# Performance work log

Hardware: AMD Instinct MI355X
Metric: run time of the kernel (lower is better)

The kernel has to match this reference:

```python
import math
import jax, jax.numpy as jnp
import numpy as np

NUM_HEADS = 8
FACTOR = 5


def setup_inputs() -> dict:
    key = jax.random.key(0)
    ks = jax.random.split(key, 5)
    B, S, D = 8, 2048, 512
    s = 1.0 / math.sqrt(D)
    return {
        "x": jax.random.normal(ks[0], (B, S, D), dtype=jnp.float32),
        "wq": jax.random.normal(ks[1], (D, D), dtype=jnp.float32) * s,
        "bq": jnp.zeros((D,), jnp.float32),
        "wk": jax.random.normal(ks[2], (D, D), dtype=jnp.float32) * s,
        "bk": jnp.zeros((D,), jnp.float32),
        "wv": jax.random.normal(ks[3], (D, D), dtype=jnp.float32) * s,
        "bv": jnp.zeros((D,), jnp.float32),
        "wo": jax.random.normal(ks[4], (D, D), dtype=jnp.float32) * s,
        "bo": jnp.zeros((D,), jnp.float32),
    }


def reference(x, wq, bq, wk, bk, wv, bv, wo, bo):
    B, S, Dm = x.shape
    H = NUM_HEADS
    Dh = Dm // H
    scale = jnp.sqrt(jnp.float32(Dh))
    # u = min(factor * ceil(ln(S)), S); S is static so compute in Python
    u = min(FACTOR * int(math.ceil(math.log(S))), S)

    def split_heads(t):  # [B,S,Dm] -> [B,H,S,Dh]
        return t.reshape(B, S, H, Dh).transpose(0, 2, 1, 3)

    q = split_heads(x @ wq + bq)
    k = split_heads(x @ wk + bk)
    v = split_heads(x @ wv + bv)

    # S >= 64 -> sparse branch (static decision).
    # Full logits only to compute sparsity measure M (max - mean over keys).
    logits = jnp.einsum("bhqd,bhkd->bhqk", q, k) / scale  # [B,H,S,S]
    M = jnp.max(logits, axis=-1) - jnp.mean(logits, axis=-1)  # [B,H,S]
    _, top_idx = jax.lax.top_k(M, u)  # [B,H,u]

    # Gather top-u queries and run dense attention only for them.
    q_top = jnp.take_along_axis(q, top_idx[..., None], axis=2)  # [B,H,u,Dh]
    top_logits = jnp.einsum("bhqd,bhkd->bhqk", q_top, k) / scale  # [B,H,u,S]
    top_w = jax.nn.softmax(top_logits, axis=-1)
    top_out = jnp.einsum("bhqk,bhkd->bhqd", top_w, v)  # [B,H,u,Dh]

    # Non-selected queries get the mean of V; scatter top outputs in.
    out = jnp.broadcast_to(jnp.mean(v, axis=2, keepdims=True), v.shape)
    b_idx = jnp.arange(B)[:, None, None]
    h_idx = jnp.arange(H)[None, :, None]
    out = out.at[b_idx, h_idx, top_idx].set(top_out)  # [B,H,S,Dh]

    out = out.transpose(0, 2, 1, 3).reshape(B, S, Dm)
    return out @ wo + bo
```

## Files before the change

### kernel.cpp

```cpp
#include <hip/hip_runtime.h>
#include <hip/hip_bf16.h>
#include <math.h>

#define NB 8
#define NS 2048
#define ND 512
#define NH 8
#define DHD 64
#define NU 40
#define NBH 64
#define NM 16384

typedef __attribute__((ext_vector_type(8))) short short8;
typedef __attribute__((ext_vector_type(4))) short short4v;
typedef __attribute__((ext_vector_type(4))) float f32x4;

__device__ __forceinline__ short f2bf(float f) {
  __hip_bfloat16 h = __float2bfloat16(f);
  return *reinterpret_cast<short*>(&h);
}
__device__ __forceinline__ float bf2f(short s) {
  __hip_bfloat16 h;
  *reinterpret_cast<short*>(&h) = s;
  return __bfloat162float(h);
}

__device__ __forceinline__ void gload_lds16(const short* g, short* l) {
  __builtin_amdgcn_global_load_lds(
      (const __attribute__((address_space(1))) unsigned int*)g,
      (__attribute__((address_space(3))) unsigned int*)l, 16, 0, 0);
}

__global__ void prep(const float* __restrict__ x, const float* __restrict__ w0,
                     const float* __restrict__ w1, const float* __restrict__ w2,
                     short* __restrict__ Xs, short* __restrict__ Wts) {
  if (blockIdx.x < 8192) {
    int i = blockIdx.x * 256 + threadIdx.x;
    const float4 v = *(const float4*)(x + (size_t)i * 4);
    int row = i >> 7;
    int col = (i & 127) << 2;
    float vv[4] = {v.x, v.y, v.z, v.w};
    short4v hi, lo;
#pragma unroll
    for (int j = 0; j < 4; ++j) {
      short h = f2bf(vv[j]);
      hi[j] = h;
      lo[j] = f2bf(vv[j] - bf2f(h));
    }
    *(short4v*)(Xs + (size_t)row * 1024 + col) = hi;
    *(short4v*)(Xs + (size_t)row * 1024 + 512 + col) = lo;
  } else {
    int bw = blockIdx.x - 8192;
    int y = bw >> 8;
    int bxy = bw & 255;
    const float* W = y == 0 ? w0 : y == 1 ? w1 : w2;
    short* dst = Wts + (size_t)y * 512 * 1024;
    __shared__ float tile[32][33];
    int bx = bxy & 15, by = bxy >> 4;
    int k0 = bx * 32, n0 = by * 32;
    int r = threadIdx.x >> 3, cg = (threadIdx.x & 7) * 4;
    const float4 v = *(const float4*)(W + (size_t)(k0 + r) * 512 + n0 + cg);
    tile[r][cg] = v.x; tile[r][cg + 1] = v.y; tile[r][cg + 2] = v.z; tile[r][cg + 3] = v.w;
    __syncthreads();
#pragma unroll
    for (int j = 0; j < 4; ++j) {
      int kk = cg + j;
      float f = tile[kk][r];
      short h = f2bf(f);
      dst[(size_t)(n0 + r) * 1024 + k0 + kk] = h;
      dst[(size_t)(n0 + r) * 1024 + 512 + k0 + kk] = f2bf(f - bf2f(h));
    }
  }
}

__global__ __launch_bounds__(256, 2) void qkvgemm(
    const short* __restrict__ A, const short* __restrict__ Wts,
    const float* __restrict__ bq, const float* __restrict__ bk,
    const float* __restrict__ bv, short* __restrict__ Qs,
    short* __restrict__ Ks, short* __restrict__ Vs) {
  __shared__ short As[2][128][64];
  __shared__ short Bs[2][128][64];
  const int bid = blockIdx.x;
  const int wgid = (bid & 7) * 192 + (bid >> 3);
  const int mb = wgid / 12, y = wgid % 12;
  const int m0 = mb * 128;
  const int wsel = y >> 2;
  const int n0 = (y & 3) * 128;
  const short* Wb = Wts + (size_t)wsel * 512 * 1024;
  const float* bias = wsel == 0 ? bq : wsel == 1 ? bk : bv;
  short* dstbase = wsel == 0 ? Qs : wsel == 1 ? Ks : Vs;

  const int tid = threadIdx.x;
  const int w = tid >> 6, lane = tid & 63;
  const int wm = (w >> 1) * 64, wn = (w & 1) * 64;
  const int fr = lane & 15, fk = lane >> 4;

  f32x4 acc[4][4];
  const f32x4 zz = {0.f, 0.f, 0.f, 0.f};
#pragma unroll
  for (int i = 0; i < 4; ++i)
#pragma unroll
    for (int j = 0; j < 4; ++j) acc[i][j] = zz;

  auto stage = [&](int buf, int kt) {
#pragma unroll
    for (int p = 0; p < 4; ++p) {
      int idx = (p * 4 + w) * 64 + lane;
      int r = idx >> 3, c = idx & 7;
      int cs = c ^ (r & 7);
      int sc = (cs < 4) ? (kt + cs * 8) : (512 + kt + (cs - 4) * 8);
      short* lA = &As[buf][0][0] + (p * 4 + w) * 512;
      short* lB = &Bs[buf][0][0] + (p * 4 + w) * 512;
      gload_lds16(A + (size_t)(m0 + r) * 1024 + sc, lA);
      gload_lds16(Wb + (size_t)(n0 + r) * 1024 + sc, lB);
    }
  };

  stage(0, 0);
  __syncthreads();
  for (int kt = 0; kt < 512; kt += 32) {
    int cur = (kt >> 5) & 1;
    if (kt + 32 < 512) stage(cur ^ 1, kt + 32);
    short8 ah[4], al[4], bh[4], bl[4];
#pragma unroll
    for (int mf = 0; mf < 4; ++mf) {
      int r = wm + mf * 16 + fr;
      ah[mf] = *(const short8*)&As[cur][r][(fk ^ (r & 7)) << 3];
      al[mf] = *(const short8*)&As[cur][r][((4 + fk) ^ (r & 7)) << 3];
    }
#pragma unroll
    for (int nf = 0; nf < 4; ++nf) {
      int r = wn + nf * 16 + fr;
      bh[nf] = *(const short8*)&Bs[cur][r][(fk ^ (r & 7)) << 3];
      bl[nf] = *(const short8*)&Bs[cur][r][((4 + fk) ^ (r & 7)) << 3];
    }
#pragma unroll
    for (int mf = 0; mf < 4; ++mf)
#pragma unroll
      for (int nf = 0; nf < 4; ++nf) {
        acc[mf][nf] = __builtin_amdgcn_mfma_f32_16x16x32_bf16(bh[nf], ah[mf], acc[mf][nf], 0, 0, 0);
        acc[mf][nf] = __builtin_amdgcn_mfma_f32_16x16x32_bf16(bh[nf], al[mf], acc[mf][nf], 0, 0, 0);
        acc[mf][nf] = __builtin_amdgcn_mfma_f32_16x16x32_bf16(bl[nf], ah[mf], acc[mf][nf], 0, 0, 0);
      }
    __syncthreads();
  }

#pragma unroll
  for (int mf = 0; mf < 4; ++mf) {
    int m = m0 + wm + mf * 16 + fr;
    int b = m >> 11, s = m & 2047;
#pragma unroll
    for (int nf = 0; nf < 4; ++nf) {
      int nb = n0 + wn + nf * 16 + fk * 4;
      float4 bi4 = *(const float4*)(bias + nb);
      int h = nb >> 6, dh = nb & 63;
      short* dst = dstbase + ((size_t)((b << 3) + h) * 2048 + s) * 128;
      short4v hi, lo;
      float bb[4] = {bi4.x, bi4.y, bi4.z, bi4.w};
#pragma unroll
      for (int j = 0; j < 4; ++j) {
        float v = acc[mf][nf][j] + bb[j];
        short hs = f2bf(v);
        hi[j] = hs;
        lo[j] = f2bf(v - bf2f(hs));
      }
      *(short4v*)(dst + dh) = hi;
      *(short4v*)(dst + 64 + dh) = lo;
    }
  }
}

__global__ __launch_bounds__(256) void colmeans(const short* __restrict__ K,
                                                const short* __restrict__ V,
                                                float* __restrict__ kbarf,
                                                float* __restrict__ vbarf) {
  const int bh = blockIdx.x >> 2, part = blockIdx.x & 3;
  const int c = threadIdx.x & 15;
  const int g = threadIdx.x >> 4;
  const int s0 = part * 512 + g * 32;
  const short* Kb = K + (size_t)bh * 2048 * 128;
  const short* Vb = V + (size_t)bh * 2048 * 128;
  float sk[8], sv[8];
#pragma unroll
  for (int e = 0; e < 8; ++e) { sk[e] = 0.f; sv[e] = 0.f; }
  for (int s = s0; s < s0 + 32; ++s) {
    short8 k8 = *(const short8*)(Kb + (size_t)s * 128 + c * 8);
    short8 v8 = *(const short8*)(Vb + (size_t)s * 128 + c * 8);
#pragma unroll
    for (int e = 0; e < 8; ++e) { sk[e] += bf2f(k8[e]); sv[e] += bf2f(v8[e]); }
  }
  __shared__ float rk[16][128], rv[16][128];
#pragma unroll
  for (int e = 0; e < 8; ++e) { rk[g][c * 8 + e] = sk[e]; rv[g][c * 8 + e] = sv[e]; }
  __syncthreads();
  if (threadIdx.x < 64) {
    int d = threadIdx.x;
    float a = 0.f, b2 = 0.f;
    for (int g2 = 0; g2 < 16; ++g2) {
      a += rk[g2][d] + rk[g2][64 + d];
      b2 += rv[g2][d] + rv[g2][64 + d];
    }
    atomicAdd(kbarf + bh * 64 + d, a * (1.f / 2048.f));
    atomicAdd(vbarf + bh * 64 + d, b2 * (1.f / 2048.f));
  }
}

__global__ __launch_bounds__(256, 2) void qkmax(const short* __restrict__ Qs,
                                                const short* __restrict__ Ks,
                                                const float* __restrict__ kbarf,
                                                float* __restrict__ Mval) {
  __shared__ short Kt[2][128][128];
  __shared__ float red[256];
  const int bid = blockIdx.x;
  const int wgid = (bid & 7) * 64 + (bid >> 3);
  const int bh = wgid >> 3, q0 = (wgid & 7) * 256;
  const short* Qb = Qs + ((size_t)bh * 2048 + q0) * 128;
  const short* Kb = Ks + (size_t)bh * 2048 * 128;
  const int tid = threadIdx.x, w = tid >> 6, lane = tid & 63;
  const int fr = lane & 15, fk = lane >> 4;

  short8 qf[4][2][2];
#pragma unroll
  for (int mf = 0; mf < 4; ++mf) {
    int row = w * 64 + mf * 16 + fr;
#pragma unroll
    for (int h = 0; h < 2; ++h)
#pragma unroll
      for (int k0 = 0; k0 < 2; ++k0) {
        int ch = h * 8 + k0 * 4 + fk;
        qf[mf][h][k0] = *(const short8*)(Qb + (size_t)row * 128 + ch * 8);
      }
  }

  f32x4 rmax[4];
  const f32x4 neg = {-1e30f, -1e30f, -1e30f, -1e30f};
#pragma unroll
  for (int mf = 0; mf < 4; ++mf) rmax[mf] = neg;
  const f32x4 zz = {0.f, 0.f, 0.f, 0.f};

  auto stageK = [&](int buf, int t) {
#pragma unroll
    for (int p = 0; p < 8; ++p) {
      int idx = (p * 4 + w) * 64 + lane;
      int r = idx >> 4, c = idx & 15;
      int cs = c ^ (r & 15);
      short* lb = &Kt[buf][0][0] + (p * 4 + w) * 512;
      gload_lds16(Kb + (size_t)(t * 128 + r) * 128 + cs * 8, lb);
    }
  };

  stageK(0, 0);
  __syncthreads();
  for (int t = 0; t < 16; ++t) {
    int cur = t & 1;
    if (t < 15) stageK(cur ^ 1, t + 1);
#pragma unroll
    for (int nf = 0; nf < 8; ++nf) {
      int r = nf * 16 + fr;
      short8 kfh[2], kfl[2];
#pragma unroll
      for (int k0 = 0; k0 < 2; ++k0) {
        kfh[k0] = *(const short8*)&Kt[cur][r][((k0 * 4 + fk) ^ (r & 15)) << 3];
        kfl[k0] = *(const short8*)&Kt[cur][r][((8 + k0 * 4 + fk) ^ (r & 15)) << 3];
      }
#pragma unroll
      for (int mf = 0; mf < 4; ++mf) {
        f32x4 a = zz;
#pragma unroll
        for (int k0 = 0; k0 < 2; ++k0) {
          a = __builtin_amdgcn_mfma_f32_16x16x32_bf16(qf[mf][0][k0], kfh[k0], a, 0, 0, 0);
          a = __builtin_amdgcn_mfma_f32_16x16x32_bf16(qf[mf][0][k0], kfl[k0], a, 0, 0, 0);
          a = __builtin_amdgcn_mfma_f32_16x16x32_bf16(qf[mf][1][k0], kfh[k0], a, 0, 0, 0);
        }
#pragma unroll
        for (int j = 0; j < 4; ++j) rmax[mf][j] = fmaxf(rmax[mf][j], a[j]);
      }
    }
    __syncthreads();
  }

#pragma unroll
  for (int mf = 0; mf < 4; ++mf)
#pragma unroll
    for (int j = 0; j < 4; ++j) {
      float r = rmax[mf][j];
      r = fmaxf(r, __shfl_xor(r, 1, 64));
      r = fmaxf(r, __shfl_xor(r, 2, 64));
      r = fmaxf(r, __shfl_xor(r, 4, 64));
      r = fmaxf(r, __shfl_xor(r, 8, 64));
      if (fr == 0) red[w * 64 + mf * 16 + fk * 4 + j] = r;
    }
  __syncthreads();

  {
    const short* qp = Qs + ((size_t)bh * 2048 + q0 + tid) * 128;
    const float* kb = kbarf + bh * 64;
    float dot = 0.f;
#pragma unroll
    for (int ch = 0; ch < 8; ++ch) {
      short8 hi = *(const short8*)(qp + ch * 8);
      short8 lo = *(const short8*)(qp + 64 + ch * 8);
#pragma unroll
      for (int e = 0; e < 8; ++e) dot += (bf2f(hi[e]) + bf2f(lo[e])) * kb[ch * 8 + e];
    }
    Mval[(size_t)bh * 2048 + q0 + tid] = (red[tid] - dot) * 0.125f;
  }
}

__global__ __launch_bounds__(256) void topk40(const float* __restrict__ Mval,
                                              int* __restrict__ tidx) {
  __shared__ float vals[4][32][64];
  const int w = threadIdx.x >> 6, lane = threadIdx.x & 63;
  const int bh = blockIdx.x * 4 + w;
  const float* src = Mval + (size_t)bh * 2048;
#pragma unroll
  for (int j = 0; j < 32; ++j) vals[w][j][lane] = src[j * 64 + lane];

  for (int it = 0; it < NU; ++it) {
    float best = -INFINITY;
    int bi = 1 << 30;
#pragma unroll
    for (int j = 0; j < 32; ++j) {
      float x = vals[w][j][lane];
      int idx = j * 64 + lane;
      if (x > best) { best = x; bi = idx; }
    }
#pragma unroll
    for (int off = 1; off < 64; off <<= 1) {
      float ov = __shfl_xor(best, off, 64);
      int oi = __shfl_xor(bi, off, 64);
      if (ov > best || (ov == best && oi < bi)) { best = ov; bi = oi; }
    }
    if (lane == 0) tidx[bh * NU + it] = bi;
    if ((bi & 63) == lane) vals[w][bi >> 6][lane] = -INFINITY;
  }
}

__global__ __launch_bounds__(256) void topattn1(const short* __restrict__ Qs,
                                                const short* __restrict__ Ks,
                                                const short* __restrict__ Vs,
                                                const int* __restrict__ topidx,
                                                float* __restrict__ pacc,
                                                float* __restrict__ pm,
                                                float* __restrict__ pl) {
  __shared__ float qs[40][68];
  __shared__ float Kst[64][132];
  __shared__ float Vsh[128][68];
  __shared__ float st[40][132];
  __shared__ float m_s[40], l_s[40], r_s[40];
  __shared__ int tix[40];
  const int tid = threadIdx.x;
  const int bh = blockIdx.x, kc = blockIdx.y;
  const short* Kb = Ks + (size_t)bh * 2048 * 128;
  const short* Vb = Vs + (size_t)bh * 2048 * 128;

  if (tid < 40) {
    tix[tid] = topidx[bh * NU + tid];
    m_s[tid] = -INFINITY;
    l_s[tid] = 0.f;
  }
  __syncthreads();
  for (int i = tid; i < 40 * 64; i += 256) {
    int q = i >> 6, dd2 = i & 63;
    const short* qp = Qs + ((size_t)bh * 2048 + tix[q]) * 128;
    qs[q][dd2] = bf2f(qp[dd2]) + bf2f(qp[64 + dd2]);
  }
  const int tx = tid & 31, ty = tid >> 5;
  const int d = tid & 63, qb = tid >> 6;
  float acc[10];
#pragma unroll
  for (int j = 0; j < 10; ++j) acc[j] = 0.f;
  __syncthreads();

  for (int t = 0; t < 4; ++t) {
    int krow0 = kc * 512 + t * 128;
#pragma unroll
    for (int p = 0; p < 4; ++p) {
      int idx = tid + (p << 8);
      int r = idx >> 3, cg = (idx & 7) << 3;
      const short8 kh = *(const short8*)(Kb + (size_t)(krow0 + r) * 128 + cg);
      const short8 kl = *(const short8*)(Kb + (size_t)(krow0 + r) * 128 + 64 + cg);
      const short8 vh = *(const short8*)(Vb + (size_t)(krow0 + r) * 128 + cg);
      const short8 vl = *(const short8*)(Vb + (size_t)(krow0 + r) * 128 + 64 + cg);
#pragma unroll
      for (int j = 0; j < 8; ++j) {
        Kst[cg + j][r] = bf2f(kh[j]) + bf2f(kl[j]);
        Vsh[r][cg + j] = bf2f(vh[j]) + bf2f(vl[j]);
      }
    }
    __syncthreads();

    {
      float c5[5][4];
#pragma unroll
      for (int i = 0; i < 5; ++i)
#pragma unroll
        for (int j = 0; j < 4; ++j) c5[i][j] = 0.f;
      for (int dd = 0; dd < 64; ++dd) {
        const float4 b4 = *(const float4*)&Kst[dd][tx << 2];
#pragma unroll
        for (int i = 0; i < 5; ++i) {
          float a = qs[ty * 5 + i][dd];
          c5[i][0] = fmaf(a, b4.x, c5[i][0]);
          c5[i][1] = fmaf(a, b4.y, c5[i][1]);
          c5[i][2] = fmaf(a, b4.z, c5[i][2]);
          c5[i][3] = fmaf(a, b4.w, c5[i][3]);
        }
      }
#pragma unroll
      for (int i = 0; i < 5; ++i) {
        float4 o;
        o.x = c5[i][0] * 0.125f; o.y = c5[i][1] * 0.125f;
        o.z = c5[i][2] * 0.125f; o.w = c5[i][3] * 0.125f;
        *(float4*)&st[ty * 5 + i][tx << 2] = o;
      }
    }
    __syncthreads();

    if (tid < 160) {
      int q = tid >> 2, sub = tid & 3;
      float tm = -INFINITY;
#pragma unroll
      for (int kk = 0; kk < 32; ++kk) tm = fmaxf(tm, st[q][sub * 32 + kk]);
      tm = fmaxf(tm, __shfl_xor(tm, 1, 64));
      tm = fmaxf(tm, __shfl_xor(tm, 2, 64));
      float mold = m_s[q];
      float mnew = fmaxf(mold, tm);
      float sum = 0.f;
#pragma unroll
      for (int kk = 0; kk < 32; ++kk) {
        float ww = __expf(st[q][sub * 32 + kk] - mnew);
        st[q][sub * 32 + kk] = ww;
        sum += ww;
      }
      sum += __shfl_xor(sum, 1, 64);
      sum += __shfl_xor(sum, 2, 64);
      if (sub == 0) {
        float r = __expf(mold - mnew);
        l_s[q] = l_s[q] * r + sum;
        m_s[q] = mnew;
        r_s[q] = r;
      }
    }
    __syncthreads();

#pragma unroll
    for (int j = 0; j < 10; ++j) {
      int q = qb + (j << 2);
      float a = 0.f;
#pragma unroll
      for (int kk = 0; kk < 128; kk += 4) {
        float4 ww = *(const float4*)&st[q][kk];
        a = fmaf(ww.x, Vsh[kk + 0][d], a);
        a = fmaf(ww.y, Vsh[kk + 1][d], a);
        a = fmaf(ww.z, Vsh[kk + 2][d], a);
        a = fmaf(ww.w, Vsh[kk + 3][d], a);
      }
      acc[j] = acc[j] * r_s[q] + a;
    }
    __syncthreads();
  }

  int pcb = bh * 4 + kc;
#pragma unroll
  for (int j = 0; j < 10; ++j) {
    int q = qb + (j << 2);
    pacc[((size_t)pcb * NU + q) * 64 + d] = acc[j];
  }
  if (tid < 40) {
    pm[pcb * NU + tid] = m_s[tid];
    pl[pcb * NU + tid] = l_s[tid];
  }
}

__global__ __launch_bounds__(256) void topcombine(const float* __restrict__ pacc,
                                                  const float* __restrict__ pm,
                                                  const float* __restrict__ pl,
                                                  float* __restrict__ tout,
                                                  const float* __restrict__ vbarf,
                                                  const float* __restrict__ Wo,
                                                  const float* __restrict__ bo,
                                                  float* __restrict__ om) {
  if (blockIdx.x < 64) {
    const int bh = blockIdx.x;
    const int d = threadIdx.x & 63, qb = threadIdx.x >> 6;
#pragma unroll
    for (int j = 0; j < 10; ++j) {
      int q = qb + (j << 2);
      float m0 = pm[(bh * 4 + 0) * NU + q], m1 = pm[(bh * 4 + 1) * NU + q];
      float m2 = pm[(bh * 4 + 2) * NU + q], m3 = pm[(bh * 4 + 3) * NU + q];
      float mx = fmaxf(fmaxf(m0, m1), fmaxf(m2, m3));
      float e0 = __expf(m0 - mx), e1 = __expf(m1 - mx);
      float e2 = __expf(m2 - mx), e3 = __expf(m3 - mx);
      float L = pl[(bh * 4 + 0) * NU + q] * e0 + pl[(bh * 4 + 1) * NU + q] * e1 +
                pl[(bh * 4 + 2) * NU + q] * e2 + pl[(bh * 4 + 3) * NU + q] * e3;
      float o = (pacc[((size_t)(bh * 4 + 0) * NU + q) * 64 + d] * e0 +
                 pacc[((size_t)(bh * 4 + 1) * NU + q) * 64 + d] * e1 +
                 pacc[((size_t)(bh * 4 + 2) * NU + q) * 64 + d] * e2 +
                 pacc[((size_t)(bh * 4 + 3) * NU + q) * 64 + d] * e3) / L;
      tout[((size_t)bh * NU + q) * 64 + d] = o;
    }
  } else {
    __shared__ float mred[4][64];
    int blk2 = blockIdx.x - 64;
    int b = blk2 >> 3, n0 = (blk2 & 7) * 64;
    int n = n0 + (threadIdx.x & 63), kq = threadIdx.x >> 6;
    const float* vb = vbarf + b * 512;
    float acc = 0.f;
#pragma unroll 8
    for (int k = kq * 128; k < kq * 128 + 128; ++k)
      acc = fmaf(vb[k], Wo[(size_t)k * 512 + n], acc);
    mred[kq][threadIdx.x & 63] = acc;
    __syncthreads();
    if (kq == 0)
      om[b * 512 + n] = bo[n] + mred[0][n - n0] + mred[1][n - n0] +
                        mred[2][n - n0] + mred[3][n - n0];
  }
}

__global__ void fillout(const float* __restrict__ om, float* __restrict__ out) {
  const size_t n4 = (size_t)NM * 128;
  for (size_t i = (size_t)blockIdx.x * 256 + threadIdx.x; i < n4;
       i += (size_t)gridDim.x * 256) {
    int m = (int)(i >> 7), c4 = (int)(i & 127) << 2;
    int b = m >> 11;
    *(float4*)(out + (size_t)m * 512 + c4) = *(const float4*)(om + b * 512 + c4);
  }
}

__global__ __launch_bounds__(256) void deltaout(const float* __restrict__ tout,
                                                const float* __restrict__ vbarf,
                                                const int* __restrict__ tidx,
                                                const float* __restrict__ Wo,
                                                float* __restrict__ out) {
  const int g = blockIdx.x;
  const int bh = g / 40;
  const int b = bh >> 3, h = bh & 7;
  const int s = tidx[g];
  __shared__ float dsh[64];
  if (threadIdx.x < 64)
    dsh[threadIdx.x] = tout[(size_t)g * 64 + threadIdx.x] - vbarf[bh * 64 + threadIdx.x];
  __syncthreads();
  const int n = threadIdx.x;
  float a0 = 0.f, a1 = 0.f;
#pragma unroll 8
  for (int dh = 0; dh < 64; ++dh) {
    float d = dsh[dh];
    const float* wrow = Wo + (size_t)(h * 64 + dh) * 512;
    a0 = fmaf(d, wrow[n], a0);
    a1 = fmaf(d, wrow[n + 256], a1);
  }
  float* orow = out + ((size_t)b * 2048 + s) * 512;
  atomicAdd(orow + n, a0);
  atomicAdd(orow + n + 256, a1);
}

extern "C" void kernel_launch(void* const* d_in, const int* in_sizes, int n_in,
                              void* d_out, int out_size, void* d_ws, size_t ws_size,
                              hipStream_t stream) {
  (void)in_sizes; (void)n_in; (void)out_size; (void)ws_size;
  const float* x  = (const float*)d_in[0];
  const float* wq = (const float*)d_in[1];
  const float* bq = (const float*)d_in[2];
  const float* wk = (const float*)d_in[3];
  const float* bk = (const float*)d_in[4];
  const float* wv = (const float*)d_in[5];
  const float* bv = (const float*)d_in[6];
  const float* wo = (const float*)d_in[7];
  const float* bo = (const float*)d_in[8];
  float* out = (float*)d_out;

  short* Xs   = (short*)d_ws;
  short* Wts  = Xs + (size_t)16384 * 1024;
  short* Qsb  = Wts + (size_t)3 * 512 * 1024;
  short* Ksb  = Qsb + (size_t)NBH * NS * 128;
  short* Vsb  = Ksb + (size_t)NBH * NS * 128;
  float* Mval = (float*)(Vsb + (size_t)NBH * NS * 128);
  float* kbarf = Mval + (size_t)NBH * NS;
  float* vbarf = kbarf + NBH * 64;
  int* tidx   = (int*)(vbarf + NBH * 64);
  float* pacc = (float*)(tidx + NBH * NU);
  float* pm   = pacc + (size_t)NBH * 4 * NU * 64;
  float* pl   = pm + NBH * 4 * NU;
  float* tout = pl + NBH * 4 * NU;
  float* om   = tout + (size_t)NBH * NU * 64;

  hipMemsetAsync(kbarf, 0, 2 * NBH * 64 * sizeof(float), stream);
  prep<<<8960, 256, 0, stream>>>(x, wq, wk, wv, Xs, Wts);
  qkvgemm<<<1536, 256, 0, stream>>>(Xs, Wts, bq, bk, bv, Qsb, Ksb, Vsb);
  colmeans<<<NBH * 4, 256, 0, stream>>>(Ksb, Vsb, kbarf, vbarf);
  qkmax<<<512, 256, 0, stream>>>(Qsb, Ksb, kbarf, Mval);
  topk40<<<16, 256, 0, stream>>>(Mval, tidx);
  topattn1<<<dim3(NBH, 4), 256, 0, stream>>>(Qsb, Ksb, Vsb, tidx, pacc, pm, pl);
  topcombine<<<128, 256, 0, stream>>>(pacc, pm, pl, tout, vbarf, wo, bo, om);
  fillout<<<2048, 256, 0, stream>>>(om, out);
  deltaout<<<NBH * NU, 256, 0, stream>>>(tout, vbarf, tidx, wo, out);
}
```

Measured before the change: 338.4 us.

## Enlarge QKV GEMM tiles and add deeper async prefetch pipelines

The QKV projection GEMM moves from 128x128 tiles with 256 threads to 256x256 tiles with 512 threads, so each operand tile loaded into LDS is reused across more output. The GEMM and the qkmax kernel now prefetch two tiles ahead with explicit vmcnt waits and raw barriers, replacing the single-stage prefetch with __syncthreads. MFMA sections are wrapped in raised wave priority. The larger tiles raise register and LDS use (64KB LDS, 128 accumulator registers per lane) and give fewer workgroups (384), which may cut occupancy and leave a tail on the GPU.

```diff
diff --git a/kernel.cpp b/kernel.cpp
--- a/kernel.cpp
+++ b/kernel.cpp
@@ -73,87 +73,100 @@
   }
 }
 
-__global__ __launch_bounds__(256, 2) void qkvgemm(
+__global__ __launch_bounds__(512, 2) void qkvgemm(
     const short* __restrict__ A, const short* __restrict__ Wts,
     const float* __restrict__ bq, const float* __restrict__ bk,
     const float* __restrict__ bv, short* __restrict__ Qs,
     short* __restrict__ Ks, short* __restrict__ Vs) {
-  __shared__ short As[2][128][64];
-  __shared__ short Bs[2][128][64];
+  __shared__ short As[2][256][64];
+  __shared__ short Bs[2][256][64];
   const int bid = blockIdx.x;
-  const int wgid = (bid & 7) * 192 + (bid >> 3);
-  const int mb = wgid / 12, y = wgid % 12;
-  const int m0 = mb * 128;
-  const int wsel = y >> 2;
-  const int n0 = (y & 3) * 128;
+  const int wgid = (bid & 7) * 48 + (bid >> 3);
+  const int mb = wgid / 6, y = wgid % 6;
+  const int m0 = mb * 256;
+  const int wsel = y >> 1;
+  const int n0 = (y & 1) * 256;
   const short* Wb = Wts + (size_t)wsel * 512 * 1024;
   const float* bias = wsel == 0 ? bq : wsel == 1 ? bk : bv;
   short* dstbase = wsel == 0 ? Qs : wsel == 1 ? Ks : Vs;
 
   const int tid = threadIdx.x;
   const int w = tid >> 6, lane = tid & 63;
-  const int wm = (w >> 1) * 64, wn = (w & 1) * 64;
+  const int wm = (w >> 2) * 128, wn = (w & 3) * 64;
   const int fr = lane & 15, fk = lane >> 4;
 
-  f32x4 acc[4][4];
+  f32x4 acc[8][4];
   const f32x4 zz = {0.f, 0.f, 0.f, 0.f};
 #pragma unroll
-  for (int i = 0; i < 4; ++i)
+  for (int i = 0; i < 8; ++i)
 #pragma unroll
     for (int j = 0; j < 4; ++j) acc[i][j] = zz;
 
-  auto stage = [&](int buf, int kt) {
+  auto stage = [&](int buf, int t) {
+    const int kt = t * 32;
 #pragma unroll
     for (int p = 0; p < 4; ++p) {
-      int idx = (p * 4 + w) * 64 + lane;
+      int idx = p * 512 + tid;
       int r = idx >> 3, c = idx & 7;
       int cs = c ^ (r & 7);
       int sc = (cs < 4) ? (kt + cs * 8) : (512 + kt + (cs - 4) * 8);
-      short* lA = &As[buf][0][0] + (p * 4 + w) * 512;
-      short* lB = &Bs[buf][0][0] + (p * 4 + w) * 512;
+      short* lA = &As[buf][0][0] + (size_t)(p * 512 + w * 64) * 8;
+      short* lB = &Bs[buf][0][0] + (size_t)(p * 512 + w * 64) * 8;
       gload_lds16(A + (size_t)(m0 + r) * 1024 + sc, lA);
       gload_lds16(Wb + (size_t)(n0 + r) * 1024 + sc, lB);
     }
   };
 
   stage(0, 0);
-  __syncthreads();
-  for (int kt = 0; kt < 512; kt += 32) {
-    int cur = (kt >> 5) & 1;
-    if (kt + 32 < 512) stage(cur ^ 1, kt + 32);
-    short8 ah[4], al[4], bh[4], bl[4];
-#pragma unroll
-    for (int mf = 0; mf < 4; ++mf) {
+  stage(1, 1);
+  for (int t = 0; t < 16; ++t) {
+    const int cur = t & 1;
+    if (t < 15) {
+      asm volatile("s_waitcnt vmcnt(8)" ::: "memory");
+    } else {
+      asm volatile("s_waitcnt vmcnt(0)" ::: "memory");
+    }
+    __builtin_amdgcn_s_barrier();
+
+    short8 af[8][2], bf[4][2];
+#pragma unroll
+    for (int mf = 0; mf < 8; ++mf) {
       int r = wm + mf * 16 + fr;
-      ah[mf] = *(const short8*)&As[cur][r][(fk ^ (r & 7)) << 3];
-      al[mf] = *(const short8*)&As[cur][r][((4 + fk) ^ (r & 7)) << 3];
+#pragma unroll
+      for (int h = 0; h < 2; ++h)
+        af[mf][h] = *(const short8*)&As[cur][r][((h * 4 + fk) ^ (r & 7)) << 3];
     }
 #pragma unroll
     for (int nf = 0; nf < 4; ++nf) {
       int r = wn + nf * 16 + fr;
-      bh[nf] = *(const short8*)&Bs[cur][r][(fk ^ (r & 7)) << 3];
-      bl[nf] = *(const short8*)&Bs[cur][r][((4 + fk) ^ (r & 7)) << 3];
-    }
-#pragma unroll
-    for (int mf = 0; mf < 4; ++mf)
-#pragma unroll
-      for (int nf = 0; nf < 4; ++nf) {
-        acc[mf][nf] = __builtin_amdgcn_mfma_f32_16x16x32_bf16(bh[nf], ah[mf], acc[mf][nf], 0, 0, 0);
-        acc[mf][nf] = __builtin_amdgcn_mfma_f32_16x16x32_bf16(bh[nf], al[mf], acc[mf][nf], 0, 0, 0);
-        acc[mf][nf] = __builtin_amdgcn_mfma_f32_16x16x32_bf16(bl[nf], ah[mf], acc[mf][nf], 0, 0, 0);
-      }
-    __syncthreads();
-  }
-
-#pragma unroll
-  for (int mf = 0; mf < 4; ++mf) {
+#pragma unroll
+      for (int h = 0; h < 2; ++h)
+        bf[nf][h] = *(const short8*)&Bs[cur][r][((h * 4 + fk) ^ (r & 7)) << 3];
+    }
+    __builtin_amdgcn_s_setprio(1);
+#pragma unroll
+    for (int nf = 0; nf < 4; ++nf)
+#pragma unroll
+      for (int mf = 0; mf < 8; ++mf) {
+        acc[mf][nf] = __builtin_amdgcn_mfma_f32_16x16x32_bf16(bf[nf][0], af[mf][0], acc[mf][nf], 0, 0, 0);
+        acc[mf][nf] = __builtin_amdgcn_mfma_f32_16x16x32_bf16(bf[nf][0], af[mf][1], acc[mf][nf], 0, 0, 0);
+        acc[mf][nf] = __builtin_amdgcn_mfma_f32_16x16x32_bf16(bf[nf][1], af[mf][0], acc[mf][nf], 0, 0, 0);
+      }
+    __builtin_amdgcn_s_setprio(0);
+    __builtin_amdgcn_sched_barrier(0);
+    __builtin_amdgcn_s_barrier();
+    if (t < 14) stage(cur, t + 2);
+  }
+
+#pragma unroll
+  for (int mf = 0; mf < 8; ++mf) {
     int m = m0 + wm + mf * 16 + fr;
     int b = m >> 11, s = m & 2047;
 #pragma unroll
     for (int nf = 0; nf < 4; ++nf) {
-      int nb = n0 + wn + nf * 16 + fk * 4;
-      float4 bi4 = *(const float4*)(bias + nb);
-      int h = nb >> 6, dh = nb & 63;
+      int nw = n0 + wn + nf * 16 + fk * 4;
+      float4 bi4 = *(const float4*)(bias + nw);
+      int h = nw >> 6, dh = nw & 63;
       short* dst = dstbase + ((size_t)((b << 3) + h) * 2048 + s) * 128;
       short4v hi, lo;
       float bb[4] = {bi4.x, bi4.y, bi4.z, bi4.w};
@@ -241,19 +254,26 @@
   auto stageK = [&](int buf, int t) {
 #pragma unroll
     for (int p = 0; p < 8; ++p) {
-      int idx = (p * 4 + w) * 64 + lane;
+      int idx = p * 256 + tid;
       int r = idx >> 4, c = idx & 15;
       int cs = c ^ (r & 15);
-      short* lb = &Kt[buf][0][0] + (p * 4 + w) * 512;
+      short* lb = &Kt[buf][0][0] + (size_t)(p * 256 + w * 64) * 8;
       gload_lds16(Kb + (size_t)(t * 128 + r) * 128 + cs * 8, lb);
     }
   };
 
   stageK(0, 0);
-  __syncthreads();
+  stageK(1, 1);
   for (int t = 0; t < 16; ++t) {
-    int cur = t & 1;
-    if (t < 15) stageK(cur ^ 1, t + 1);
+    const int cur = t & 1;
+    if (t < 15) {
+      asm volatile("s_waitcnt vmcnt(8)" ::: "memory");
+    } else {
+      asm volatile("s_waitcnt vmcnt(0)" ::: "memory");
+    }
+    __builtin_amdgcn_s_barrier();
+
+    __builtin_amdgcn_s_setprio(1);
 #pragma unroll
     for (int nf = 0; nf < 8; ++nf) {
       int r = nf * 16 + fr;
@@ -276,7 +296,10 @@
         for (int j = 0; j < 4; ++j) rmax[mf][j] = fmaxf(rmax[mf][j], a[j]);
       }
     }
-    __syncthreads();
+    __builtin_amdgcn_s_setprio(0);
+    __builtin_amdgcn_sched_barrier(0);
+    __builtin_amdgcn_s_barrier();
+    if (t < 14) stageK(cur, t + 2);
   }
 
 #pragma unroll
@@ -587,7 +610,7 @@
 
   hipMemsetAsync(kbarf, 0, 2 * NBH * 64 * sizeof(float), stream);
   prep<<<8960, 256, 0, stream>>>(x, wq, wk, wv, Xs, Wts);
-  qkvgemm<<<1536, 256, 0, stream>>>(Xs, Wts, bq, bk, bv, Qsb, Ksb, Vsb);
+  qkvgemm<<<384, 512, 0, stream>>>(Xs, Wts, bq, bk, bv, Qsb, Ksb, Vsb);
   colmeans<<<NBH * 4, 256, 0, stream>>>(Ksb, Vsb, kbarf, vbarf);
   qkmax<<<512, 256, 0, stream>>>(Qsb, Ksb, kbarf, Mval);
   topk40<<<16, 256, 0, stream>>>(Mval, tidx);
```

New measurement: 367.7 us. +8.6%, slower.

## Retile qkmax to 128-query blocks and fuse fill and delta output passes

Applied to the files above, without the earlier changes.

The qkmax kernel now handles 128 queries per block, with each wave taking a 32-key slice of every K tile; a cross-wave max reduction goes through shared memory, and the grid doubles to 1024 blocks for more parallelism. topk40 also writes a per-row, per-head slot map. A new outall kernel uses that map to write each output row once: the per-batch mean projection plus the deltas of any selected heads. This replaces the separate fill kernel and the atomic delta kernel, removing the atomics and the second pass over the output, at the cost of an extra memset for the slot map and a per-row lookup.

```diff
diff --git a/kernel.cpp b/kernel.cpp
--- a/kernel.cpp
+++ b/kernel.cpp
@@ -210,41 +210,41 @@
                                                 const float* __restrict__ kbarf,
                                                 float* __restrict__ Mval) {
   __shared__ short Kt[2][128][128];
-  __shared__ float red[256];
+  __shared__ float red[4][128];
   const int bid = blockIdx.x;
-  const int wgid = (bid & 7) * 64 + (bid >> 3);
-  const int bh = wgid >> 3, q0 = (wgid & 7) * 256;
+  const int wgid = (bid & 7) * 128 + (bid >> 3);
+  const int bh = wgid >> 4, q0 = (wgid & 15) * 128;
   const short* Qb = Qs + ((size_t)bh * 2048 + q0) * 128;
   const short* Kb = Ks + (size_t)bh * 2048 * 128;
   const int tid = threadIdx.x, w = tid >> 6, lane = tid & 63;
   const int fr = lane & 15, fk = lane >> 4;
 
-  short8 qf[4][2][2];
-#pragma unroll
-  for (int mf = 0; mf < 4; ++mf) {
-    int row = w * 64 + mf * 16 + fr;
-#pragma unroll
-    for (int h = 0; h < 2; ++h)
-#pragma unroll
-      for (int k0 = 0; k0 < 2; ++k0) {
-        int ch = h * 8 + k0 * 4 + fk;
-        qf[mf][h][k0] = *(const short8*)(Qb + (size_t)row * 128 + ch * 8);
-      }
-  }
-
-  f32x4 rmax[4];
-  const f32x4 neg = {-1e30f, -1e30f, -1e30f, -1e30f};
-#pragma unroll
-  for (int mf = 0; mf < 4; ++mf) rmax[mf] = neg;
+  short8 qf[8][2][2];
+#pragma unroll
+  for (int mf = 0; mf < 8; ++mf) {
+    int row = mf * 16 + fr;
+#pragma unroll
+    for (int hl = 0; hl < 2; ++hl)
+#pragma unroll
+      for (int k0 = 0; k0 < 2; ++k0)
+        qf[mf][hl][k0] =
+            *(const short8*)(Qb + (size_t)row * 128 + hl * 64 + k0 * 32 + fk * 8);
+  }
+
+  f32x4 rmax[8];
+#pragma unroll
+  for (int mf = 0; mf < 8; ++mf)
+#pragma unroll
+    for (int j = 0; j < 4; ++j) rmax[mf][j] = -1e30f;
   const f32x4 zz = {0.f, 0.f, 0.f, 0.f};
 
   auto stageK = [&](int buf, int t) {
 #pragma unroll
     for (int p = 0; p < 8; ++p) {
-      int idx = (p * 4 + w) * 64 + lane;
+      int idx = p * 256 + tid;
       int r = idx >> 4, c = idx & 15;
       int cs = c ^ (r & 15);
-      short* lb = &Kt[buf][0][0] + (p * 4 + w) * 512;
+      short* lb = &Kt[buf][0][0] + (size_t)(p * 256 + w * 64) * 8;
       gload_lds16(Kb + (size_t)(t * 128 + r) * 128 + cs * 8, lb);
     }
   };
@@ -252,11 +252,11 @@
   stageK(0, 0);
   __syncthreads();
   for (int t = 0; t < 16; ++t) {
-    int cur = t & 1;
+    const int cur = t & 1;
     if (t < 15) stageK(cur ^ 1, t + 1);
 #pragma unroll
-    for (int nf = 0; nf < 8; ++nf) {
-      int r = nf * 16 + fr;
+    for (int nf = 0; nf < 2; ++nf) {
+      int r = w * 32 + nf * 16 + fr;
       short8 kfh[2], kfl[2];
 #pragma unroll
       for (int k0 = 0; k0 < 2; ++k0) {
@@ -264,7 +264,7 @@
         kfl[k0] = *(const short8*)&Kt[cur][r][((8 + k0 * 4 + fk) ^ (r & 15)) << 3];
       }
 #pragma unroll
-      for (int mf = 0; mf < 4; ++mf) {
+      for (int mf = 0; mf < 8; ++mf) {
         f32x4 a = zz;
 #pragma unroll
         for (int k0 = 0; k0 < 2; ++k0) {
@@ -280,7 +280,7 @@
   }
 
 #pragma unroll
-  for (int mf = 0; mf < 4; ++mf)
+  for (int mf = 0; mf < 8; ++mf)
 #pragma unroll
     for (int j = 0; j < 4; ++j) {
       float r = rmax[mf][j];
@@ -288,12 +288,14 @@
       r = fmaxf(r, __shfl_xor(r, 2, 64));
       r = fmaxf(r, __shfl_xor(r, 4, 64));
       r = fmaxf(r, __shfl_xor(r, 8, 64));
-      if (fr == 0) red[w * 64 + mf * 16 + fk * 4 + j] = r;
+      if (fr == 0) red[w][mf * 16 + fk * 4 + j] = r;
     }
   __syncthreads();
 
-  {
-    const short* qp = Qs + ((size_t)bh * 2048 + q0 + tid) * 128;
+  if (tid < 128) {
+    float mx = fmaxf(fmaxf(red[0][tid], red[1][tid]),
+                     fmaxf(red[2][tid], red[3][tid]));
+    const short* qp = Qb + (size_t)tid * 128;
     const float* kb = kbarf + bh * 64;
     float dot = 0.f;
 #pragma unroll
@@ -303,12 +305,13 @@
 #pragma unroll
       for (int e = 0; e < 8; ++e) dot += (bf2f(hi[e]) + bf2f(lo[e])) * kb[ch * 8 + e];
     }
-    Mval[(size_t)bh * 2048 + q0 + tid] = (red[tid] - dot) * 0.125f;
+    Mval[(size_t)bh * 2048 + q0 + tid] = (mx - dot) * 0.125f;
   }
 }
 
 __global__ __launch_bounds__(256) void topk40(const float* __restrict__ Mval,
-                                              int* __restrict__ tidx) {
+                                              int* __restrict__ tidx,
+                                              int* __restrict__ slot8) {
   __shared__ float vals[4][32][64];
   const int w = threadIdx.x >> 6, lane = threadIdx.x & 63;
   const int bh = blockIdx.x * 4 + w;
@@ -331,7 +334,10 @@
       int oi = __shfl_xor(bi, off, 64);
       if (ov > best || (ov == best && oi < bi)) { best = ov; bi = oi; }
     }
-    if (lane == 0) tidx[bh * NU + it] = bi;
+    if (lane == 0) {
+      tidx[bh * NU + it] = bi;
+      slot8[((size_t)(bh >> 3) * 2048 + bi) * 8 + (bh & 7)] = it;
+    }
     if ((bi & 63) == lane) vals[w][bi >> 6][lane] = -INFINITY;
   }
 }
@@ -518,41 +524,38 @@
   }
 }
 
-__global__ void fillout(const float* __restrict__ om, float* __restrict__ out) {
-  const size_t n4 = (size_t)NM * 128;
-  for (size_t i = (size_t)blockIdx.x * 256 + threadIdx.x; i < n4;
-       i += (size_t)gridDim.x * 256) {
-    int m = (int)(i >> 7), c4 = (int)(i & 127) << 2;
-    int b = m >> 11;
-    *(float4*)(out + (size_t)m * 512 + c4) = *(const float4*)(om + b * 512 + c4);
-  }
-}
-
-__global__ __launch_bounds__(256) void deltaout(const float* __restrict__ tout,
-                                                const float* __restrict__ vbarf,
-                                                const int* __restrict__ tidx,
-                                                const float* __restrict__ Wo,
-                                                float* __restrict__ out) {
-  const int g = blockIdx.x;
-  const int bh = g / 40;
-  const int b = bh >> 3, h = bh & 7;
-  const int s = tidx[g];
+__global__ __launch_bounds__(256) void outall(const float* __restrict__ om,
+                                              const int* __restrict__ slot8,
+                                              const float* __restrict__ tout,
+                                              const float* __restrict__ vbarf,
+                                              const float* __restrict__ Wo,
+                                              float* __restrict__ out) {
+  const int r = blockIdx.x;
+  const int b = r >> 11;
+  const int n = threadIdx.x;
+  float o0 = om[b * 512 + n];
+  float o1 = om[b * 512 + n + 256];
   __shared__ float dsh[64];
-  if (threadIdx.x < 64)
-    dsh[threadIdx.x] = tout[(size_t)g * 64 + threadIdx.x] - vbarf[bh * 64 + threadIdx.x];
-  __syncthreads();
-  const int n = threadIdx.x;
-  float a0 = 0.f, a1 = 0.f;
+#pragma unroll
+  for (int h = 0; h < 8; ++h) {
+    int it = slot8[(size_t)r * 8 + h];
+    if (it >= 0) {
+      int bh = b * 8 + h;
+      int g = bh * NU + it;
+      __syncthreads();
+      if (n < 64) dsh[n] = tout[(size_t)g * 64 + n] - vbarf[bh * 64 + n];
+      __syncthreads();
 #pragma unroll 8
-  for (int dh = 0; dh < 64; ++dh) {
-    float d = dsh[dh];
-    const float* wrow = Wo + (size_t)(h * 64 + dh) * 512;
-    a0 = fmaf(d, wrow[n], a0);
-    a1 = fmaf(d, wrow[n + 256], a1);
-  }
-  float* orow = out + ((size_t)b * 2048 + s) * 512;
-  atomicAdd(orow + n, a0);
-  atomicAdd(orow + n + 256, a1);
+      for (int dh = 0; dh < 64; ++dh) {
+        float d = dsh[dh];
+        const float* wrow = Wo + (size_t)(h * 64 + dh) * 512;
+        o0 = fmaf(d, wrow[n], o0);
+        o1 = fmaf(d, wrow[n + 256], o1);
+      }
+    }
+  }
+  out[(size_t)r * 512 + n] = o0;
+  out[(size_t)r * 512 + n + 256] = o1;
 }
 
 extern "C" void kernel_launch(void* const* d_in, const int* in_sizes, int n_in,
@@ -579,20 +582,21 @@
   float* kbarf = Mval + (size_t)NBH * NS;
   float* vbarf = kbarf + NBH * 64;
   int* tidx   = (int*)(vbarf + NBH * 64);
-  float* pacc = (float*)(tidx + NBH * NU);
+  int* slot8  = tidx + NBH * NU;
+  float* pacc = (float*)(slot8 + (size_t)NM * 8);
   float* pm   = pacc + (size_t)NBH * 4 * NU * 64;
   float* pl   = pm + NBH * 4 * NU;
   float* tout = pl + NBH * 4 * NU;
   float* om   = tout + (size_t)NBH * NU * 64;
 
   hipMemsetAsync(kbarf, 0, 2 * NBH * 64 * sizeof(float), stream);
+  hipMemsetAsync(slot8, 0xFF, (size_t)NM * 8 * sizeof(int), stream);
   prep<<<8960, 256, 0, stream>>>(x, wq, wk, wv, Xs, Wts);
   qkvgemm<<<1536, 256, 0, stream>>>(Xs, Wts, bq, bk, bv, Qsb, Ksb, Vsb);
   colmeans<<<NBH * 4, 256, 0, stream>>>(Ksb, Vsb, kbarf, vbarf);
-  qkmax<<<512, 256, 0, stream>>>(Qsb, Ksb, kbarf, Mval);
-  topk40<<<16, 256, 0, stream>>>(Mval, tidx);
+  qkmax<<<1024, 256, 0, stream>>>(Qsb, Ksb, kbarf, Mval);
+  topk40<<<16, 256, 0, stream>>>(Mval, tidx, slot8);
   topattn1<<<dim3(NBH, 4), 256, 0, stream>>>(Qsb, Ksb, Vsb, tidx, pacc, pm, pl);
   topcombine<<<128, 256, 0, stream>>>(pacc, pm, pl, tout, vbarf, wo, bo, om);
-  fillout<<<2048, 256, 0, stream>>>(om, out);
-  deltaout<<<NBH * NU, 256, 0, stream>>>(tout, vbarf, tidx, wo, out);
-}
+  outall<<<NM, 256, 0, stream>>>(om, slot8, tout, vbarf, wo, out);
+}
```

After: 351.5 us. +3.9%, slower.
